# Kernel optimization log

Hardware: AMD Instinct MI355X
Metric: run time of the kernel (lower is better)

The kernel has to match this reference:

```python
import jax, jax.numpy as jnp
import numpy as np

N, D, T, ET, E = 100000, 128, 3, 4, 250000


def gru_cell(m, h, w_ih, w_hh, b_ih, b_hh):
    # torch.nn.GRUCell semantics
    gi = m @ w_ih.T + b_ih          # [N, 3D]
    gh = h @ w_hh.T + b_hh          # [N, 3D]
    i_r, i_z, i_n = jnp.split(gi, 3, axis=1)
    h_r, h_z, h_n = jnp.split(gh, 3, axis=1)
    r = jax.nn.sigmoid(i_r + h_r)
    z = jax.nn.sigmoid(i_z + h_z)
    n = jnp.tanh(i_n + r * h_n)
    return (1.0 - z) * n + z * h


def setup_inputs() -> dict:
    key = jax.random.key(0)
    ks = jax.random.split(key, 10)
    x = jax.random.normal(ks[0], (N, D), dtype=jnp.float32)
    edge_row = jax.random.randint(ks[1], (ET, E), 0, N, dtype=jnp.int32)
    edge_col = jax.random.randint(ks[2], (ET, E), 0, N, dtype=jnp.int32)
    edge_val = jnp.ones((ET, E), dtype=jnp.float32)
    xav = float(np.sqrt(6.0 / (D + D)))  # xavier_uniform per (D,D) slice
    weight = jax.random.uniform(ks[3], (T, ET, D, D), jnp.float32, -xav, xav)
    bias_w = jax.random.uniform(ks[4], (T, ET, D), jnp.float32, -0.01, 0.01)
    s = float(1.0 / np.sqrt(D))  # GRUCell default init range
    w_ih = jax.random.uniform(ks[5], (3 * D, D), jnp.float32, -s, s)
    w_hh = jax.random.uniform(ks[6], (3 * D, D), jnp.float32, -s, s)
    b_ih = jax.random.uniform(ks[7], (3 * D,), jnp.float32, -s, s)
    b_hh = jax.random.uniform(ks[8], (3 * D,), jnp.float32, -s, s)
    return {"x": x, "edge_row": edge_row, "edge_col": edge_col,
            "edge_val": edge_val, "weight": weight, "bias_w": bias_w,
            "w_ih": w_ih, "w_hh": w_hh, "b_ih": b_ih, "b_hh": b_hh}


def reference(x, edge_row, edge_col, edge_val, weight, bias_w, w_ih, w_hh, b_ih, b_hh):
    n_nodes = x.shape[0]
    h = x  # input_dim == out_channels, no zero-padding needed
    num_t = weight.shape[0]

    def agg_one(m_e, col_e, row_e, val_e):
        # sparse.mm: out[row] += val * m[col]
        msg = m_e[col_e] * val_e[:, None]                 # [E, D]
        return jax.ops.segment_sum(msg, row_e, num_segments=n_nodes)

    for t in range(num_t):
        # per-edge-type dense transform: [ET, N, D]
        m = jnp.einsum('nd,edf->enf', h, weight[t]) + bias_w[t][:, None, :]
        agg = jax.vmap(agg_one)(m, edge_col, edge_row, edge_val)  # [ET, N, D]
        m_sum = agg.sum(axis=0)                                    # [N, D]
        h = gru_cell(m_sum, h, w_ih, w_hh, b_ih, b_hh)
    return h
```

## Files before the change

kernel.cpp:

```cpp
#include <hip/hip_runtime.h>
#include <hip/hip_fp16.h>
#include <stdint.h>

#define NN  100000
#define DD  128
#define TT  3
#define ETT 4
#define EE  250000
#define NCH 49

typedef float  f32x4  __attribute__((ext_vector_type(4)));
typedef __bf16 bf16x8 __attribute__((ext_vector_type(8)));

__device__ __forceinline__ float bf2f(uint32_t u){ u <<= 16; return __builtin_bit_cast(float, u); }
__device__ __forceinline__ uint32_t f2bf(float f){
  uint32_t u = __builtin_bit_cast(uint32_t, f);
  return (u + 0x7FFFu + ((u >> 16) & 1u)) >> 16;
}
__device__ __forceinline__ float h2f(uint32_t u){ return __half2float(__ushort_as_half((uint16_t)u)); }
__device__ __forceinline__ uint32_t f2h(float f){ return (uint32_t)__half_as_ushort(__float2half(f)); }
__device__ __forceinline__ f32x4 mfma16(bf16x8 a, bf16x8 b, f32x4 c){
  return __builtin_amdgcn_mfma_f32_16x16x32_bf16(a, b, c, 0, 0, 0);
}
__device__ __forceinline__ void fmamix_lo(float& acc, uint32_t h, float v){
  asm("v_fma_mix_f32 %0, %1, %2, %0 op_sel:[0,0,0] op_sel_hi:[1,0,0]"
      : "+v"(acc) : "v"(h), "v"(v));
}
__device__ __forceinline__ void fmamix_hi(float& acc, uint32_t h, float v){
  asm("v_fma_mix_f32 %0, %1, %2, %0 op_sel:[1,0,0] op_sel_hi:[1,0,0]"
      : "+v"(acc) : "v"(h), "v"(v));
}

__global__ void k_count(const int* __restrict__ erow, const float* __restrict__ eval,
                        int* __restrict__ counts, float* __restrict__ degval){
  int idx = blockIdx.x * 256 + threadIdx.x;
  if (idx >= ETT * EE) return;
  int e = idx / EE;
  int row = erow[idx];
  atomicAdd(&counts[e * NN + row], 1);
  atomicAdd(&degval[e * NN + row], eval[idx]);
}

__global__ void k_blksum(const int* __restrict__ counts, int* __restrict__ bsum){
  const int b = blockIdx.x, e = b / NCH, c = b % NCH;
  const int* p = counts + e * NN + c * 2048;
  int lim = NN - c * 2048; if (lim > 2048) lim = 2048;
  const int t = threadIdx.x;
  int s = 0;
  #pragma unroll
  for (int i = 0; i < 8; ++i){
    int idx = i * 256 + t;
    if (idx < lim) s += p[idx];
  }
  #pragma unroll
  for (int d = 32; d; d >>= 1) s += __shfl_down(s, d);
  __shared__ int wsum[4];
  if ((t & 63) == 0) wsum[t >> 6] = s;
  __syncthreads();
  if (t == 0) bsum[b] = wsum[0] + wsum[1] + wsum[2] + wsum[3];
}

__global__ void k_scanp(const int* __restrict__ bsum, int* __restrict__ bexc,
                        int* __restrict__ offsets){
  const int t = threadIdx.x, wid = t >> 6, l = t & 63;
  int v = (l < NCH) ? bsum[wid * NCH + l] : 0;
  int x = v;
  #pragma unroll
  for (int d = 1; d < 64; d <<= 1){ int y = __shfl_up(x, d); if (l >= d) x += y; }
  if (l < NCH) bexc[wid * NCH + l] = x - v;
  if (l == NCH - 1) offsets[wid * (NN + 1) + NN] = x;
}

__global__ void k_apply(const int* __restrict__ counts, const int* __restrict__ bexc,
                        int* __restrict__ offsets){
  const int b = blockIdx.x, e = b / NCH, c = b % NCH;
  const int* p = counts + e * NN + c * 2048;
  int* off = offsets + e * (NN + 1) + c * 2048;
  int lim = NN - c * 2048; if (lim > 2048) lim = 2048;
  const int t = threadIdx.x, l = t & 63, wid = t >> 6;
  __shared__ int wt[4];
  int v[8], s = 0;
  #pragma unroll
  for (int i = 0; i < 8; ++i){
    int idx = t * 8 + i;
    v[i] = (idx < lim) ? p[idx] : 0; s += v[i];
  }
  int x = s;
  #pragma unroll
  for (int d = 1; d < 64; d <<= 1){ int y = __shfl_up(x, d); if (l >= d) x += y; }
  if (l == 63) wt[wid] = x;
  __syncthreads();
  int wexc = 0;
  #pragma unroll
  for (int k = 0; k < 4; ++k) if (k < wid) wexc += wt[k];
  int te = bexc[b] + wexc + (x - s);
  #pragma unroll
  for (int i = 0; i < 8; ++i){
    int idx = t * 8 + i;
    if (idx < lim) off[idx] = te;
    te += v[i];
  }
}

__global__ void k_fill(const int* __restrict__ erow, const int* __restrict__ ecol,
                       const float* __restrict__ eval, const int* __restrict__ offsets,
                       int* __restrict__ cursor, uint2* __restrict__ sedge){
  int idx = blockIdx.x * 256 + threadIdx.x;
  if (idx >= ETT * EE) return;
  int e = idx / EE;
  int row = erow[idx];
  int pos = atomicAdd(&cursor[e * NN + row], 1);
  int o = offsets[e * (NN + 1) + row] + pos;
  sedge[e * EE + o] = make_uint2((uint32_t)ecol[idx], __builtin_bit_cast(uint32_t, eval[idx]));
}

__global__ void k_conv_x(const float* __restrict__ x, uint16_t* __restrict__ hh){
  int idx = blockIdx.x * 256 + threadIdx.x;
  const float4* xp = (const float4*)x;
  float4 a = xp[idx * 2], b = xp[idx * 2 + 1];
  uint32_t p0 = f2h(a.x) | (f2h(a.y) << 16);
  uint32_t p1 = f2h(a.z) | (f2h(a.w) << 16);
  uint32_t p2 = f2h(b.x) | (f2h(b.y) << 16);
  uint32_t p3 = f2h(b.z) | (f2h(b.w) << 16);
  ((uint4*)hh)[idx] = make_uint4(p0, p1, p2, p3);
}

__global__ void k_conv_w(const float* __restrict__ weight, const float* __restrict__ wih,
                         const float* __restrict__ whh, const float* __restrict__ bih,
                         const float* __restrict__ bhh, uint16_t* __restrict__ wcatT,
                         uint16_t* __restrict__ wgru, float* __restrict__ bcomb){
  int idx = blockIdx.x * 256 + threadIdx.x;
  if (idx < TT * 128 * 512){
    int t = idx / 65536; int rem = idx - t * 65536;
    int f = rem >> 9; int u = rem & 511;
    int e = u >> 7; int d = u & 127;
    wcatT[idx] = (uint16_t)f2bf(weight[(((t * 4 + e) * 128 + d) << 7) + f]);
  }
  if (idx < 192 * 512){
    const int frag = idx >> 9, within = idx & 511;
    const int lane = within >> 3, i = within & 7;
    const int ks = frag & 3, bb = (frag >> 2) & 1, m = (frag >> 3) & 1;
    const int rem2 = frag >> 4;
    const int g = rem2 % 3, w = rem2 / 3;
    const int j = g * 128 + w * 32 + bb * 16 + (lane & 15);
    const int k = ks * 32 + (lane >> 4) * 8 + i;
    const float* src = m ? whh : wih;
    wgru[idx] = (uint16_t)f2bf(src[j * 128 + k]);
  }
  if (idx < 256) bcomb[idx] = bih[idx] + bhh[idx];
}

#define HACC8(val, u, base) \
  fmamix_lo(acc[base+0], u.x, val); fmamix_hi(acc[base+1], u.x, val); \
  fmamix_lo(acc[base+2], u.y, val); fmamix_hi(acc[base+3], u.y, val); \
  fmamix_lo(acc[base+4], u.z, val); fmamix_hi(acc[base+5], u.z, val); \
  fmamix_lo(acc[base+6], u.w, val); fmamix_hi(acc[base+7], u.w, val);

__global__ __launch_bounds__(256, 4) void k_step(
    const uint16_t* __restrict__ hsrc, uint16_t* __restrict__ hdst,
    float* __restrict__ out_f32, int last,
    const int* __restrict__ offsets, const uint2* __restrict__ sedge,
    const float* __restrict__ degval, const float* __restrict__ bias_w,
    const uint16_t* __restrict__ wcatT_t, int tstep,
    const uint16_t* __restrict__ wgru, const float* __restrict__ bcomb,
    const float* __restrict__ b_ih, const float* __restrict__ b_hh)
{
  __shared__ uint16_t aggT[32 * 512];
  __shared__ uint4 shB[512];
  const int tid = threadIdx.x;
  const int node0 = blockIdx.x * 32;

  {
    const int nl = tid >> 3, q = tid & 7;
    const int n = node0 + nl;
    #pragma unroll
    for (int e = 0; e < ETT; ++e){
      float acc[16];
      #pragma unroll
      for (int i = 0; i < 16; ++i) acc[i] = 0.f;
      const int s  = offsets[e * (NN + 1) + n];
      const int en = offsets[e * (NN + 1) + n + 1];
      const uint2* ep = sedge + (size_t)e * EE;
      #pragma unroll 1
      for (int i = s; i < en; i += 6){
        const int lastI = en - 1;
        uint2 cv[6]; float vv[6];
        #pragma unroll
        for (int j = 0; j < 6; ++j){
          const int k = i + j;
          const int kc = (k < lastI) ? k : lastI;
          cv[j] = ep[kc];
          vv[j] = (k <= lastI) ? __builtin_bit_cast(float, cv[j].y) : 0.f;
        }
        uint4 ua[6], ub[6];
        #pragma unroll
        for (int j = 0; j < 6; ++j){
          const uint4* p = (const uint4*)(hsrc + (size_t)cv[j].x * DD + q * 16);
          ua[j] = p[0]; ub[j] = p[1];
        }
        #pragma unroll
        for (int j = 0; j < 6; ++j){
          const float v = vv[j];
          HACC8(v, ua[j], 0); HACC8(v, ub[j], 8);
        }
      }
      #pragma unroll
      for (int c2 = 0; c2 < 2; ++c2){
        const int c  = e * 16 + q * 2 + c2;
        const int cs = c ^ (nl & 7);
        uint32_t p0 = f2bf(acc[c2*8+0]) | (f2bf(acc[c2*8+1]) << 16);
        uint32_t p1 = f2bf(acc[c2*8+2]) | (f2bf(acc[c2*8+3]) << 16);
        uint32_t p2 = f2bf(acc[c2*8+4]) | (f2bf(acc[c2*8+5]) << 16);
        uint32_t p3 = f2bf(acc[c2*8+6]) | (f2bf(acc[c2*8+7]) << 16);
        *(uint4*)&aggT[nl * 512 + cs * 8] = make_uint4(p0, p1, p2, p3);
      }
    }
  }
  __syncthreads();

  const int lane = tid & 63, w = tid >> 6;
  const int rlo = lane & 15, kg = lane >> 4;

  #pragma unroll
  for (int i = 0; i < 2; ++i){
    const int slot = tid * 2 + i;
    const int sn = slot >> 4, scs = slot & 15;
    const int sc = scs ^ (sn & 7);
    const uint4 hr = *(const uint4*)(hsrc + (size_t)(node0 + sn) * DD + sc * 8);
    uint32_t r0 = f2bf(h2f(hr.x & 0xffffu)) | (f2bf(h2f(hr.x >> 16)) << 16);
    uint32_t r1 = f2bf(h2f(hr.y & 0xffffu)) | (f2bf(h2f(hr.y >> 16)) << 16);
    uint32_t r2 = f2bf(h2f(hr.z & 0xffffu)) | (f2bf(h2f(hr.z >> 16)) << 16);
    uint32_t r3 = f2bf(h2f(hr.w & 0xffffu)) | (f2bf(h2f(hr.w >> 16)) << 16);
    shB[slot] = make_uint4(r0, r1, r2, r3);
  }

  const int rt = w & 1, fh = w >> 1;
  const int rowA = rt * 16 + rlo;
  f32x4 C[4];
  #pragma unroll
  for (int i = 0; i < 4; ++i) C[i] = f32x4{0.f, 0.f, 0.f, 0.f};

  #pragma unroll
  for (int ks = 0; ks < 16; ++ks){
    const int cs = (ks * 4 + kg) ^ (rowA & 7);
    bf16x8 a = __builtin_bit_cast(bf16x8, *(const uint4*)&aggT[rowA * 512 + cs * 8]);
    #pragma unroll
    for (int ft = 0; ft < 4; ++ft){
      const int f = fh * 64 + ft * 16 + rlo;
      bf16x8 b = __builtin_bit_cast(bf16x8, *(const uint4*)(wcatT_t + (size_t)f * 512 + ks * 32 + kg * 8));
      C[ft] = mfma16(a, b, C[ft]);
    }
  }

  const float* bwt = bias_w + tstep * (ETT * DD);
  float dv[4][4];
  #pragma unroll
  for (int r = 0; r < 4; ++r){
    const int n2 = node0 + rt * 16 + kg * 4 + r;
    #pragma unroll
    for (int e = 0; e < 4; ++e) dv[e][r] = degval[e * NN + n2];
  }
  __syncthreads();

  uint16_t* mT = aggT;
  #pragma unroll
  for (int ft = 0; ft < 4; ++ft){
    const int f = fh * 64 + ft * 16 + rlo;
    const float b0 = bwt[f], b1 = bwt[128 + f], b2 = bwt[256 + f], b3 = bwt[384 + f];
    #pragma unroll
    for (int r = 0; r < 4; ++r){
      const int n2l = rt * 16 + kg * 4 + r;
      const float bias = dv[0][r]*b0 + dv[1][r]*b1 + dv[2][r]*b2 + dv[3][r]*b3;
      mT[n2l * 128 + (((f >> 3) ^ (n2l & 7)) << 3) + (f & 7)] = (uint16_t)f2bf(C[ft][r] + bias);
    }
  }
  __syncthreads();

  const uint4* mT4 = (const uint4*)aggT;
  #pragma unroll
  for (int bb = 0; bb < 2; ++bb){
    f32x4 acc[3][2][2];
    #pragma unroll
    for (int g = 0; g < 3; ++g)
      #pragma unroll
      for (int m = 0; m < 2; ++m)
        #pragma unroll
        for (int ns = 0; ns < 2; ++ns) acc[g][m][ns] = f32x4{0.f,0.f,0.f,0.f};

    #pragma unroll
    for (int ks = 0; ks < 4; ++ks){
      bf16x8 fa[3], fb[3];
      #pragma unroll
      for (int g = 0; g < 3; ++g){
        const int fragA = (((w * 3 + g) * 2 + 0) * 2 + bb) * 4 + ks;
        const int fragB = (((w * 3 + g) * 2 + 1) * 2 + bb) * 4 + ks;
        fa[g] = __builtin_bit_cast(bf16x8, *(const uint4*)(wgru + fragA * 512 + lane * 8));
        fb[g] = __builtin_bit_cast(bf16x8, *(const uint4*)(wgru + fragB * 512 + lane * 8));
      }
      #pragma unroll
      for (int ns = 0; ns < 2; ++ns){
        const int node = ns * 16 + rlo;
        const int cs = (ks * 4 + kg) ^ (node & 7);
        const bf16x8 bm = __builtin_bit_cast(bf16x8, mT4[node * 16 + cs]);
        const bf16x8 bh = __builtin_bit_cast(bf16x8, shB[node * 16 + cs]);
        #pragma unroll
        for (int g = 0; g < 3; ++g){
          acc[g][0][ns] = mfma16(fa[g], bm, acc[g][0][ns]);
          acc[g][1][ns] = mfma16(fb[g], bh, acc[g][1][ns]);
        }
      }
    }

    const int d0 = w * 32 + bb * 16 + kg * 4;
    const f32x4 brz = *(const f32x4*)(bcomb + d0);
    const f32x4 bzz = *(const f32x4*)(bcomb + 128 + d0);
    const f32x4 bin = *(const f32x4*)(b_ih + 256 + d0);
    const f32x4 bhn = *(const f32x4*)(b_hh + 256 + d0);
    #pragma unroll
    for (int ns = 0; ns < 2; ++ns){
      const int node = node0 + ns * 16 + rlo;
      const uint2 hov = *(const uint2*)(hsrc + (size_t)node * DD + d0);
      const float ho[4] = { h2f(hov.x & 0xffffu), h2f(hov.x >> 16),
                            h2f(hov.y & 0xffffu), h2f(hov.y >> 16) };
      float hv[4];
      #pragma unroll
      for (int r = 0; r < 4; ++r){
        const float rg = 1.f / (1.f + __expf(-(acc[0][0][ns][r] + acc[0][1][ns][r] + brz[r])));
        const float zg = 1.f / (1.f + __expf(-(acc[1][0][ns][r] + acc[1][1][ns][r] + bzz[r])));
        const float xa = (acc[2][0][ns][r] + bin[r]) + rg * (acc[2][1][ns][r] + bhn[r]);
        const float ng = 1.f - 2.f / (__expf(2.f * xa) + 1.f);
        hv[r] = (1.f - zg) * ng + zg * ho[r];
      }
      if (last){
        *(f32x4*)(out_f32 + (size_t)node * DD + d0) = f32x4{hv[0], hv[1], hv[2], hv[3]};
      } else {
        uint32_t q0 = f2h(hv[0]) | (f2h(hv[1]) << 16);
        uint32_t q1 = f2h(hv[2]) | (f2h(hv[3]) << 16);
        *(uint2*)(hdst + (size_t)node * DD + d0) = make_uint2(q0, q1);
      }
    }
  }
}

extern "C" void kernel_launch(void* const* d_in, const int* in_sizes, int n_in,
                              void* d_out, int out_size, void* d_ws, size_t ws_size,
                              hipStream_t stream) {
  const float* x      = (const float*)d_in[0];
  const int*   erow   = (const int*)d_in[1];
  const int*   ecol   = (const int*)d_in[2];
  const float* eval   = (const float*)d_in[3];
  const float* weight = (const float*)d_in[4];
  const float* bias_w = (const float*)d_in[5];
  const float* wih    = (const float*)d_in[6];
  const float* whh    = (const float*)d_in[7];
  const float* bih    = (const float*)d_in[8];
  const float* bhh    = (const float*)d_in[9];
  float* out = (float*)d_out;
  char* ws = (char*)d_ws;

  size_t o = 0;
  auto alloc = [&](size_t bytes)->char*{ char* p = ws + o; o += (bytes + 255) & ~(size_t)255; return p; };
  int*      counts  = (int*)     alloc((size_t)ETT * NN * 4);
  int*      cursor  = (int*)     alloc((size_t)ETT * NN * 4);
  float*    degval  = (float*)   alloc((size_t)ETT * NN * 4);
  int*      offsets = (int*)     alloc((size_t)ETT * (NN + 1) * 4);
  int*      bsum    = (int*)     alloc((size_t)ETT * NCH * 4);
  int*      bexc    = (int*)     alloc((size_t)ETT * NCH * 4);
  uint2*    sedge   = (uint2*)   alloc((size_t)ETT * EE * 8);
  uint16_t* hh0     = (uint16_t*)alloc((size_t)NN * DD * 2);
  uint16_t* hh1     = (uint16_t*)alloc((size_t)NN * DD * 2);
  uint16_t* wcatT   = (uint16_t*)alloc((size_t)TT * 128 * 512 * 2);
  uint16_t* wgru    = (uint16_t*)alloc((size_t)192 * 512 * 2);
  float*    bcomb   = (float*)   alloc((size_t)256 * 4);
  (void)ws_size; (void)in_sizes; (void)n_in; (void)out_size;

  hipMemsetAsync(counts, 0, (size_t)3 * ETT * NN * 4, stream);

  k_count<<<(ETT * EE + 255) / 256, 256, 0, stream>>>(erow, eval, counts, degval);
  k_blksum<<<ETT * NCH, 256, 0, stream>>>(counts, bsum);
  k_scanp<<<1, 256, 0, stream>>>(bsum, bexc, offsets);
  k_apply<<<ETT * NCH, 256, 0, stream>>>(counts, bexc, offsets);
  k_fill<<<(ETT * EE + 255) / 256, 256, 0, stream>>>(erow, ecol, eval, offsets, cursor, sedge);
  k_conv_x<<<(NN * DD / 8) / 256, 256, 0, stream>>>(x, hh0);
  k_conv_w<<<(TT * 128 * 512 + 255) / 256, 256, 0, stream>>>(weight, wih, whh, bih, bhh,
                                                             wcatT, wgru, bcomb);

  uint16_t* hs = hh0;
  uint16_t* hd = hh1;
  for (int t = 0; t < TT; ++t){
    const int last = (t == TT - 1);
    k_step<<<NN / 32, 256, 0, stream>>>(hs, hd, out, last, offsets, sedge, degval,
                                        bias_w, wcatT + (size_t)t * 65536, t,
                                        wgru, bcomb, bih, bhh);
    uint16_t* tmp = hs; hs = hd; hd = tmp;
  }
}
```

Measured before the change: 675.0 us.

## Fuse preprocessing kernels and stage GRU output through LDS for coalesced stores

Merges the scan-partials kernel into the apply kernel: each block recomputes its own exclusive prefix from the block sums, and the last block writes the total offset. The degree-value atomic moves from the count pass into the fill pass, and the x and weight conversion kernels merge into one launch. In the step kernel, the fp16 hidden-state output is staged through shared memory with a swizzle so each thread writes full 16-byte rows instead of scattered 8-byte stores. The aim is fewer launches and better-coalesced global writes, at the cost of an extra barrier and LDS traffic per step.

```diff
diff --git a/kernel.cpp b/kernel.cpp
--- a/kernel.cpp
+++ b/kernel.cpp
@@ -31,14 +31,11 @@
       : "+v"(acc) : "v"(h), "v"(v));
 }
 
-__global__ void k_count(const int* __restrict__ erow, const float* __restrict__ eval,
-                        int* __restrict__ counts, float* __restrict__ degval){
+__global__ void k_count(const int* __restrict__ erow, int* __restrict__ counts){
   int idx = blockIdx.x * 256 + threadIdx.x;
   if (idx >= ETT * EE) return;
   int e = idx / EE;
-  int row = erow[idx];
-  atomicAdd(&counts[e * NN + row], 1);
-  atomicAdd(&degval[e * NN + row], eval[idx]);
+  atomicAdd(&counts[e * NN + erow[idx]], 1);
 }
 
 __global__ void k_blksum(const int* __restrict__ counts, int* __restrict__ bsum){
@@ -60,18 +57,7 @@
   if (t == 0) bsum[b] = wsum[0] + wsum[1] + wsum[2] + wsum[3];
 }
 
-__global__ void k_scanp(const int* __restrict__ bsum, int* __restrict__ bexc,
-                        int* __restrict__ offsets){
-  const int t = threadIdx.x, wid = t >> 6, l = t & 63;
-  int v = (l < NCH) ? bsum[wid * NCH + l] : 0;
-  int x = v;
-  #pragma unroll
-  for (int d = 1; d < 64; d <<= 1){ int y = __shfl_up(x, d); if (l >= d) x += y; }
-  if (l < NCH) bexc[wid * NCH + l] = x - v;
-  if (l == NCH - 1) offsets[wid * (NN + 1) + NN] = x;
-}
-
-__global__ void k_apply(const int* __restrict__ counts, const int* __restrict__ bexc,
+__global__ void k_apply(const int* __restrict__ counts, const int* __restrict__ bsum,
                         int* __restrict__ offsets){
   const int b = blockIdx.x, e = b / NCH, c = b % NCH;
   const int* p = counts + e * NN + c * 2048;
@@ -79,6 +65,13 @@
   int lim = NN - c * 2048; if (lim > 2048) lim = 2048;
   const int t = threadIdx.x, l = t & 63, wid = t >> 6;
   __shared__ int wt[4];
+  __shared__ int s_bexc;
+  if (wid == 0){
+    int vb = (l < c) ? bsum[e * NCH + l] : 0;
+    #pragma unroll
+    for (int d = 32; d; d >>= 1) vb += __shfl_down(vb, d);
+    if (l == 0) s_bexc = vb;
+  }
   int v[8], s = 0;
   #pragma unroll
   for (int i = 0; i < 8; ++i){
@@ -93,43 +86,47 @@
   int wexc = 0;
   #pragma unroll
   for (int k = 0; k < 4; ++k) if (k < wid) wexc += wt[k];
-  int te = bexc[b] + wexc + (x - s);
+  int te = s_bexc + wexc + (x - s);
   #pragma unroll
   for (int i = 0; i < 8; ++i){
     int idx = t * 8 + i;
     if (idx < lim) off[idx] = te;
     te += v[i];
   }
+  if (c == NCH - 1 && t == 0)
+    offsets[e * (NN + 1) + NN] = s_bexc + wt[0] + wt[1] + wt[2] + wt[3];
 }
 
 __global__ void k_fill(const int* __restrict__ erow, const int* __restrict__ ecol,
                        const float* __restrict__ eval, const int* __restrict__ offsets,
-                       int* __restrict__ cursor, uint2* __restrict__ sedge){
+                       int* __restrict__ cursor, uint2* __restrict__ sedge,
+                       float* __restrict__ degval){
   int idx = blockIdx.x * 256 + threadIdx.x;
   if (idx >= ETT * EE) return;
   int e = idx / EE;
   int row = erow[idx];
+  float v = eval[idx];
   int pos = atomicAdd(&cursor[e * NN + row], 1);
   int o = offsets[e * (NN + 1) + row] + pos;
-  sedge[e * EE + o] = make_uint2((uint32_t)ecol[idx], __builtin_bit_cast(uint32_t, eval[idx]));
-}
-
-__global__ void k_conv_x(const float* __restrict__ x, uint16_t* __restrict__ hh){
+  sedge[e * EE + o] = make_uint2((uint32_t)ecol[idx], __builtin_bit_cast(uint32_t, v));
+  atomicAdd(&degval[e * NN + row], v);
+}
+
+__global__ void k_conv(const float* __restrict__ x, const float* __restrict__ weight,
+                       const float* __restrict__ wih, const float* __restrict__ whh,
+                       const float* __restrict__ bih, const float* __restrict__ bhh,
+                       uint16_t* __restrict__ hh, uint16_t* __restrict__ wcatT,
+                       uint16_t* __restrict__ wgru, float* __restrict__ bcomb){
   int idx = blockIdx.x * 256 + threadIdx.x;
-  const float4* xp = (const float4*)x;
-  float4 a = xp[idx * 2], b = xp[idx * 2 + 1];
-  uint32_t p0 = f2h(a.x) | (f2h(a.y) << 16);
-  uint32_t p1 = f2h(a.z) | (f2h(a.w) << 16);
-  uint32_t p2 = f2h(b.x) | (f2h(b.y) << 16);
-  uint32_t p3 = f2h(b.z) | (f2h(b.w) << 16);
-  ((uint4*)hh)[idx] = make_uint4(p0, p1, p2, p3);
-}
-
-__global__ void k_conv_w(const float* __restrict__ weight, const float* __restrict__ wih,
-                         const float* __restrict__ whh, const float* __restrict__ bih,
-                         const float* __restrict__ bhh, uint16_t* __restrict__ wcatT,
-                         uint16_t* __restrict__ wgru, float* __restrict__ bcomb){
-  int idx = blockIdx.x * 256 + threadIdx.x;
+  if (idx < NN * DD / 8){
+    const float4* xp = (const float4*)x;
+    float4 a = xp[idx * 2], b = xp[idx * 2 + 1];
+    uint32_t p0 = f2h(a.x) | (f2h(a.y) << 16);
+    uint32_t p1 = f2h(a.z) | (f2h(a.w) << 16);
+    uint32_t p2 = f2h(b.x) | (f2h(b.y) << 16);
+    uint32_t p3 = f2h(b.z) | (f2h(b.w) << 16);
+    ((uint4*)hh)[idx] = make_uint4(p0, p1, p2, p3);
+  }
   if (idx < TT * 128 * 512){
     int t = idx / 65536; int rem = idx - t * 65536;
     int f = rem >> 9; int u = rem & 511;
@@ -277,6 +274,7 @@
   __syncthreads();
 
   const uint4* mT4 = (const uint4*)aggT;
+  uint2 qv[2][2];
   #pragma unroll
   for (int bb = 0; bb < 2; ++bb){
     f32x4 acc[3][2][2];
@@ -334,10 +332,32 @@
       if (last){
         *(f32x4*)(out_f32 + (size_t)node * DD + d0) = f32x4{hv[0], hv[1], hv[2], hv[3]};
       } else {
-        uint32_t q0 = f2h(hv[0]) | (f2h(hv[1]) << 16);
-        uint32_t q1 = f2h(hv[2]) | (f2h(hv[3]) << 16);
-        *(uint2*)(hdst + (size_t)node * DD + d0) = make_uint2(q0, q1);
-      }
+        qv[bb][ns] = make_uint2(f2h(hv[0]) | (f2h(hv[1]) << 16),
+                                f2h(hv[2]) | (f2h(hv[3]) << 16));
+      }
+    }
+  }
+
+  if (!last){
+    __syncthreads();
+    uint16_t* oT = (uint16_t*)shB;
+    #pragma unroll
+    for (int bb = 0; bb < 2; ++bb){
+      #pragma unroll
+      for (int ns = 0; ns < 2; ++ns){
+        const int node = ns * 16 + rlo;
+        const int cw  = w * 4 + bb * 2 + (kg >> 1);
+        const int cws = cw ^ (node & 7);
+        *(uint2*)((char*)oT + node * 256 + cws * 16 + (kg & 1) * 8) = qv[bb][ns];
+      }
+    }
+    __syncthreads();
+    #pragma unroll
+    for (int i = 0; i < 2; ++i){
+      const int slot = tid * 2 + i;
+      const int sn = slot >> 4, p = slot & 15;
+      const uint4 val = *(const uint4*)((char*)oT + sn * 256 + (p ^ (sn & 7)) * 16);
+      *(uint4*)(hdst + (size_t)(node0 + sn) * DD + p * 8) = val;
     }
   }
 }
@@ -365,7 +385,6 @@
   float*    degval  = (float*)   alloc((size_t)ETT * NN * 4);
   int*      offsets = (int*)     alloc((size_t)ETT * (NN + 1) * 4);
   int*      bsum    = (int*)     alloc((size_t)ETT * NCH * 4);
-  int*      bexc    = (int*)     alloc((size_t)ETT * NCH * 4);
   uint2*    sedge   = (uint2*)   alloc((size_t)ETT * EE * 8);
   uint16_t* hh0     = (uint16_t*)alloc((size_t)NN * DD * 2);
   uint16_t* hh1     = (uint16_t*)alloc((size_t)NN * DD * 2);
@@ -376,14 +395,13 @@
 
   hipMemsetAsync(counts, 0, (size_t)3 * ETT * NN * 4, stream);
 
-  k_count<<<(ETT * EE + 255) / 256, 256, 0, stream>>>(erow, eval, counts, degval);
+  k_count<<<(ETT * EE + 255) / 256, 256, 0, stream>>>(erow, counts);
   k_blksum<<<ETT * NCH, 256, 0, stream>>>(counts, bsum);
-  k_scanp<<<1, 256, 0, stream>>>(bsum, bexc, offsets);
-  k_apply<<<ETT * NCH, 256, 0, stream>>>(counts, bexc, offsets);
-  k_fill<<<(ETT * EE + 255) / 256, 256, 0, stream>>>(erow, ecol, eval, offsets, cursor, sedge);
-  k_conv_x<<<(NN * DD / 8) / 256, 256, 0, stream>>>(x, hh0);
-  k_conv_w<<<(TT * 128 * 512 + 255) / 256, 256, 0, stream>>>(weight, wih, whh, bih, bhh,
-                                                             wcatT, wgru, bcomb);
+  k_apply<<<ETT * NCH, 256, 0, stream>>>(counts, bsum, offsets);
+  k_fill<<<(ETT * EE + 255) / 256, 256, 0, stream>>>(erow, ecol, eval, offsets,
+                                                     cursor, sedge, degval);
+  k_conv<<<(NN * DD / 8 + 255) / 256, 256, 0, stream>>>(x, weight, wih, whh, bih, bhh,
+                                                        hh0, wcatT, wgru, bcomb);
 
   uint16_t* hs = hh0;
   uint16_t* hd = hh1;
```

New measurement: 682.8 us. Within noise of the previous version (+1.2%).
